# Kernel tuning notes

Hardware: AMD Instinct MI355X
Metric: run time of the kernel (lower is better)

Reference implementation:

```python
import jax, jax.numpy as jnp
import numpy as np

D_MODEL = 1024
NUM_HEADS = 16
HEAD_DIM = D_MODEL // NUM_HEADS  # 64


def setup_inputs() -> dict:
    key = jax.random.key(0)
    k1, k2, k3 = jax.random.split(key, 3)
    x = jax.random.normal(k1, (4, 2048, D_MODEL), dtype=jnp.float32)
    w_qkv = jax.random.normal(k2, (3 * D_MODEL, D_MODEL), dtype=jnp.float32) * 0.02
    b_qkv = jnp.zeros((3 * D_MODEL,), dtype=jnp.float32)
    w_out = jax.random.normal(k3, (D_MODEL, D_MODEL), dtype=jnp.float32) * 0.02
    b_out = jnp.zeros((D_MODEL,), dtype=jnp.float32)
    return {"x": x, "w_qkv": w_qkv, "b_qkv": b_qkv, "w_out": w_out, "b_out": b_out}


def reference(x, w_qkv, b_qkv, w_out, b_out):
    N, S, _ = x.shape
    # qkv projection: (N, S, 3*D) -> (3, N, heads, S, head_dim), matching torch permute(2,0,3,1,4)
    qkv = (jnp.einsum('nsd,ed->nse', x, w_qkv) + b_qkv)
    qkv = qkv.reshape(N, S, 3, NUM_HEADS, HEAD_DIM).transpose(2, 0, 3, 1, 4)
    queries, keys, values = qkv[0], qkv[1], qkv[2]  # each (N, heads, S, head_dim)
    # Faithful to source: einsum labels axis1 as 'q'/'k' and axis2 as 'h',
    # so energy has shape (N, S, heads, heads) -- attention over the heads axis.
    energy = jnp.einsum('nqhd,nkhd->nhqk', queries, keys)
    attention = jax.nn.softmax(energy / jnp.sqrt(jnp.float32(HEAD_DIM)), axis=3)
    out = jnp.einsum('nhql,nlhd->nqhd', attention, values).reshape(N, S, D_MODEL)
    return jnp.einsum('nsd,od->nso', out, w_out) + b_out
```

## Files before the change

### kernel.cpp

```cpp
#include <hip/hip_runtime.h>
#include <hip/hip_bf16.h>


typedef __hip_bfloat16 bf16;
using bf16x8 = __attribute__((ext_vector_type(8))) short;
using f32x4  = __attribute__((ext_vector_type(4))) float;

__device__ __forceinline__ float b2f(unsigned short u) {
    return __uint_as_float(((unsigned)u) << 16);
}
__device__ __forceinline__ unsigned short f2b(float f) {
    bf16 h = __float2bfloat16(f);
    return *reinterpret_cast<unsigned short*>(&h);
}
__device__ __forceinline__ void store1(float* p, float v) { *p = v; }
__device__ __forceinline__ void store1(bf16* p, float v) { *p = __float2bfloat16(v); }

__device__ __forceinline__ void gload_lds16(const bf16* g, bf16* l) {
    __builtin_amdgcn_global_load_lds(
        (const __attribute__((address_space(1))) void*)g,
        (__attribute__((address_space(3))) void*)l, 16, 0, 0);
}

#define BAR()   __builtin_amdgcn_s_barrier()
#define LGKM(N) asm volatile("s_waitcnt lgkmcnt(" #N ")" ::: "memory")
#define VMC(N)  asm volatile("s_waitcnt vmcnt(" #N ")" ::: "memory")

template <typename CT>
__global__ __launch_bounds__(512, 2)
void gemm1b(const bf16* __restrict__ A, const bf16* __restrict__ B,
            const float* __restrict__ bias, CT* __restrict__ C,
            int M, int N, int K, int gx) {
    __shared__ alignas(1024) bf16 smem[3][384 * 64];

    const int t    = threadIdx.x;
    const int lane = t & 63;
    const int wid  = t >> 6;
    const int wr   = wid >> 2;
    const int wc   = wid & 3;

    const int nwg = gridDim.x;
    const int bid = blockIdx.x;
    const int wg  = (bid & 7) * (nwg >> 3) + (bid >> 3);
    const int m0  = (wg / gx) * 128;
    const int n0  = (wg % gx) * 256;

    const int nt = K / 64;

    const int srow = lane >> 3;
    const int kel  = ((lane & 7) ^ (lane >> 3)) * 8;

    auto stageA = [&](int tt) {
        if (tt >= nt) return;
        bf16* lp = &smem[tt % 3][wid * 1024];
        const bf16* gp = A + (size_t)(m0 + wid * 16 + srow) * K + tt * 64 + kel;
        gload_lds16(gp, lp);
        gload_lds16(gp + (size_t)8 * K, lp + 512);
    };
    auto stageB = [&](int tt, int h) {
        if (tt >= nt) return;
        bf16* lp = &smem[tt % 3][8192 + h * 8192 + wid * 1024];
        const bf16* gp = B + (size_t)(n0 + h * 128 + wid * 16 + srow) * K + tt * 64 + kel;
        gload_lds16(gp, lp);
        gload_lds16(gp + (size_t)8 * K, lp + 512);
    };

    const int arow_base = wr * 64 + (lane & 15);
    const int brow_base = wc * 64 + (lane & 15);
    const int kqb       = (lane >> 4) * 16;
    auto LDA = [&](int buf, int kk, int m) -> bf16x8 {
        const int row = arow_base + m * 16;
        const int ab  = row * 128 + ((kk * 64 + kqb) ^ ((row & 7) << 4));
        return *(const bf16x8*)((const char*)&smem[buf][0] + ab);
    };
    auto LDB = [&](int buf, int kk, int n) -> bf16x8 {
        const int row = brow_base + n * 16;
        const int bb  = 16384 + row * 128 + ((kk * 64 + kqb) ^ ((row & 7) << 4));
        return *(const bf16x8*)((const char*)&smem[buf][0] + bb);
    };

    f32x4 acc[4][4] = {};
    bf16x8 af0[4], bf0[4], af1[4], bf1[4];

    stageA(0); stageB(0, 0); stageB(0, 1);
    stageA(1); stageB(1, 0); stageB(1, 1);
    VMC(6);
    BAR();

    for (int tt = 0; tt < nt; ++tt) {
        const int buf = tt % 3;

#pragma unroll
        for (int m = 0; m < 4; ++m) af0[m] = LDA(buf, 0, m);
#pragma unroll
        for (int n = 0; n < 4; ++n) bf0[n] = LDB(buf, 0, n);
#pragma unroll
        for (int m = 0; m < 4; ++m) af1[m] = LDA(buf, 1, m);
#pragma unroll
        for (int n = 0; n < 4; ++n) bf1[n] = LDB(buf, 1, n);
        stageA(tt + 2); stageB(tt + 2, 0); stageB(tt + 2, 1);
        LGKM(8);
        __builtin_amdgcn_s_setprio(1);
#pragma unroll
        for (int m = 0; m < 4; ++m)
#pragma unroll
            for (int n = 0; n < 4; ++n)
                acc[m][n] = __builtin_amdgcn_mfma_f32_16x16x32_bf16(
                    af0[m], bf0[n], acc[m][n], 0, 0, 0);
        __builtin_amdgcn_s_setprio(0);
        LGKM(0);
        __builtin_amdgcn_s_setprio(1);
#pragma unroll
        for (int m = 0; m < 4; ++m)
#pragma unroll
            for (int n = 0; n < 4; ++n)
                acc[m][n] = __builtin_amdgcn_mfma_f32_16x16x32_bf16(
                    af1[m], bf1[n], acc[m][n], 0, 0, 0);
        __builtin_amdgcn_s_setprio(0);
        if (tt < nt - 2) { VMC(6); } else { VMC(0); }
        BAR();
    }

#pragma unroll
    for (int m = 0; m < 4; ++m) {
        const int row = m0 + wr * 64 + m * 16 + (lane >> 4) * 4;
#pragma unroll
        for (int n = 0; n < 4; ++n) {
            const int col = n0 + wc * 64 + n * 16 + (lane & 15);
            const float bval = bias[col];
#pragma unroll
            for (int r = 0; r < 4; ++r)
                store1(&C[(size_t)(row + r) * N + col], acc[m][n][r] + bval);
        }
    }
}

__global__ __launch_bounds__(256)
void cvt2_f32_bf16(const float* __restrict__ in1, bf16* __restrict__ out1, int n1,
                   const float* __restrict__ in2, bf16* __restrict__ out2, int n2) {
    int i = blockIdx.x * 256 + threadIdx.x;
    const float* in;
    bf16* out;
    if (i < n1) { in = in1; out = out1; }
    else        { in = in2; out = out2; i -= n1; if (i >= n2) return; }
    float4 v = ((const float4*)in)[i];
    ushort4 o = {f2b(v.x), f2b(v.y), f2b(v.z), f2b(v.w)};
    ((ushort4*)out)[i] = o;
}

__global__ __launch_bounds__(256)
void cvt_f32_bf16(const float* __restrict__ in, bf16* __restrict__ out, int n4) {
    int i = blockIdx.x * 256 + threadIdx.x;
    if (i >= n4) return;
    float4 v = ((const float4*)in)[i];
    ushort4 o = {f2b(v.x), f2b(v.y), f2b(v.z), f2b(v.w)};
    ((ushort4*)out)[i] = o;
}

__global__ __launch_bounds__(256)
void attn_kernel(const bf16* __restrict__ qkv, bf16* __restrict__ T) {
    __shared__ float lds[4][48 * 68];

    const int wave = threadIdx.x >> 6;
    const int lane = threadIdx.x & 63;
    const int token = blockIdx.x * 4 + wave;
    const int n = token >> 11;
    const int s = token & 2047;

    float* L = lds[wave];
    const bf16* src = qkv + (size_t)token * 3072;

#pragma unroll
    for (int i = 0; i < 6; ++i) {
        int idx = i * 64 + lane;
        uint4 v = *reinterpret_cast<const uint4*>(src + (size_t)idx * 8);
        int e0 = idx * 8;
        float* dst = &L[(e0 >> 6) * 68 + (e0 & 63)];
        float4 a, b;
        a.x = b2f((unsigned short)(v.x & 0xffff));
        a.y = b2f((unsigned short)(v.x >> 16));
        a.z = b2f((unsigned short)(v.y & 0xffff));
        a.w = b2f((unsigned short)(v.y >> 16));
        b.x = b2f((unsigned short)(v.z & 0xffff));
        b.y = b2f((unsigned short)(v.z >> 16));
        b.z = b2f((unsigned short)(v.w & 0xffff));
        b.w = b2f((unsigned short)(v.w >> 16));
        *(float4*)dst = a;
        *(float4*)(dst + 4) = b;
    }
    __syncthreads();

    const int q0 = lane & 15;
    const int g  = lane >> 4;

    float e[4] = {0.f, 0.f, 0.f, 0.f};
    const float* Qr = &L[q0 * 68];
    const float* K0 = &L[(16 + g * 4) * 68];
#pragma unroll
    for (int d = 0; d < 64; d += 4) {
        float4 q4 = *(const float4*)(Qr + d);
#pragma unroll
        for (int j = 0; j < 4; ++j) {
            float4 k4 = *(const float4*)(K0 + j * 68 + d);
            e[j] += q4.x * k4.x + q4.y * k4.y + q4.z * k4.z + q4.w * k4.w;
        }
    }
#pragma unroll
    for (int j = 0; j < 4; ++j) e[j] *= 0.125f;

    float m = fmaxf(fmaxf(e[0], e[1]), fmaxf(e[2], e[3]));
    m = fmaxf(m, __shfl_xor(m, 16));
    m = fmaxf(m, __shfl_xor(m, 32));
    float p[4], sum = 0.f;
#pragma unroll
    for (int j = 0; j < 4; ++j) { p[j] = __expf(e[j] - m); sum += p[j]; }
    sum += __shfl_xor(sum, 16);
    sum += __shfl_xor(sum, 32);
    const float inv = 1.0f / sum;

    float prow[16];
#pragma unroll
    for (int j = 0; j < 4; ++j) {
        prow[g * 4 + j]         = p[j] * inv;
        prow[((g ^ 1) * 4) + j] = __shfl_xor(p[j], 16) * inv;
        prow[((g ^ 2) * 4) + j] = __shfl_xor(p[j], 32) * inv;
        prow[((g ^ 3) * 4) + j] = __shfl_xor(p[j], 48) * inv;
    }

    const int d0 = g * 16;
    float4 o4[4] = {};
#pragma unroll
    for (int k = 0; k < 16; ++k) {
        const float p1 = prow[k];
        const float* Vr = &L[(32 + k) * 68 + d0];
#pragma unroll
        for (int c = 0; c < 4; ++c) {
            float4 v = *(const float4*)(Vr + c * 4);
            o4[c].x += p1 * v.x; o4[c].y += p1 * v.y;
            o4[c].z += p1 * v.z; o4[c].w += p1 * v.w;
        }
    }
    unsigned short outv[16];
#pragma unroll
    for (int c = 0; c < 4; ++c) {
        outv[c * 4 + 0] = f2b(o4[c].x); outv[c * 4 + 1] = f2b(o4[c].y);
        outv[c * 4 + 2] = f2b(o4[c].z); outv[c * 4 + 3] = f2b(o4[c].w);
    }
    const int sp = q0 * 128 + (s >> 4);
    size_t off = ((size_t)n * 2048 + sp) * 1024 + (size_t)(s & 15) * 64 + d0;
    uint4* dst = reinterpret_cast<uint4*>(T + off);
    const uint4* sv = reinterpret_cast<const uint4*>(outv);
    dst[0] = sv[0];
    dst[1] = sv[1];
}

extern "C" void kernel_launch(void* const* d_in, const int* in_sizes, int n_in,
                              void* d_out, int out_size, void* d_ws, size_t ws_size,
                              hipStream_t stream) {
    const float* x     = (const float*)d_in[0];
    const float* w_qkv = (const float*)d_in[1];
    const float* b_qkv = (const float*)d_in[2];
    const float* w_out = (const float*)d_in[3];
    const float* b_out = (const float*)d_in[4];
    float* out = (float*)d_out;

    const int M = 8192, E = 3072, K = 1024, D = 1024;

    bf16* qkv = (bf16*)d_ws;
    bf16* T   = qkv + (size_t)M * E;
    bf16* W2b = qkv;
    bf16* W1b = (bf16*)d_out;
    bf16* X16 = W1b + (size_t)E * K;

    dim3 blk(256);
    const int n1 = M * K / 4, n2 = E * K / 4;

    cvt2_f32_bf16<<<dim3((n1 + n2) / 256), blk, 0, stream>>>(
        x, X16, n1, w_qkv, W1b, n2);
    gemm1b<bf16><<<dim3((M / 128) * (E / 256)), dim3(512), 0, stream>>>(
        X16, W1b, b_qkv, qkv, M, E, K, E / 256);
    attn_kernel<<<dim3(M / 4), blk, 0, stream>>>(qkv, T);
    cvt_f32_bf16<<<dim3(D * K / 4 / 256), blk, 0, stream>>>(w_out, W2b, D * K / 4);
    gemm1b<float><<<dim3((M / 128) * (D / 256)), dim3(512), 0, stream>>>(
        T, W2b, b_out, out, M, D, K, D / 256);
}
```

Measured before the change: 124.1 us.

## Add 128x384 tile GEMM kernel for the QKV projection

Adds a dedicated GEMM kernel with a 128x384 output tile and two-stage LDS double buffering, and uses it for the QKV projection in place of the 128x256 triple-buffered kernel. Each wave now computes a 64x96 sub-tile (4x6 MFMA blocks), which raises arithmetic intensity per LDS load and cuts the block count from 768 to 512. The cost is 128KB of LDS per block and more accumulator registers. With 512 blocks on 256 CUs the work divides into even waves, but occupancy may fall, and the shallower pipeline exposes more load latency.

```diff
diff --git a/kernel.cpp b/kernel.cpp
--- a/kernel.cpp
+++ b/kernel.cpp
@@ -25,6 +25,116 @@
 #define BAR()   __builtin_amdgcn_s_barrier()
 #define LGKM(N) asm volatile("s_waitcnt lgkmcnt(" #N ")" ::: "memory")
 #define VMC(N)  asm volatile("s_waitcnt vmcnt(" #N ")" ::: "memory")
+
+__global__ __launch_bounds__(512, 2)
+void gemm384(const bf16* __restrict__ A, const bf16* __restrict__ B,
+             const float* __restrict__ bias, bf16* __restrict__ C,
+             int M, int N, int K, int gx) {
+    __shared__ alignas(1024) bf16 smem[2][512 * 64];
+
+    const int t    = threadIdx.x;
+    const int lane = t & 63;
+    const int wid  = t >> 6;
+    const int wr   = wid >> 2;
+    const int wc   = wid & 3;
+
+    const int nwg = gridDim.x;
+    const int bid = blockIdx.x;
+    const int wg  = (bid & 7) * (nwg >> 3) + (bid >> 3);
+    const int m0  = (wg / gx) * 128;
+    const int n0  = (wg % gx) * 384;
+    const int nt  = K / 64;
+
+    const int srow = lane >> 3;
+    const int kel  = ((lane & 7) ^ (lane >> 3)) * 8;
+
+    auto stageA = [&](int tt) {
+        if (tt >= nt) return;
+        bf16* lp = &smem[tt & 1][wid * 1024];
+        const bf16* gp = A + (size_t)(m0 + wid * 16 + srow) * K + tt * 64 + kel;
+        gload_lds16(gp, lp);
+        gload_lds16(gp + (size_t)8 * K, lp + 512);
+    };
+    auto stageB = [&](int tt) {
+        if (tt >= nt) return;
+        bf16* lp = &smem[tt & 1][8192 + wid * 3072];
+        const bf16* gp = B + (size_t)(n0 + wid * 48 + srow) * K + tt * 64 + kel;
+#pragma unroll
+        for (int i = 0; i < 6; ++i)
+            gload_lds16(gp + (size_t)(i * 8) * K, lp + i * 512);
+    };
+
+    const int arow_base = wr * 64 + (lane & 15);
+    const int brow_base = wc * 96 + (lane & 15);
+    const int kqb       = (lane >> 4) * 16;
+    auto LDA = [&](int buf, int kk, int m) -> bf16x8 {
+        const int row = arow_base + m * 16;
+        const int ab  = row * 128 + ((kk * 64 + kqb) ^ ((row & 7) << 4));
+        return *(const bf16x8*)((const char*)&smem[buf][0] + ab);
+    };
+    auto LDB = [&](int buf, int kk, int n) -> bf16x8 {
+        const int row = brow_base + n * 16;
+        const int bb  = 16384 + row * 128 + ((kk * 64 + kqb) ^ ((row & 7) << 4));
+        return *(const bf16x8*)((const char*)&smem[buf][0] + bb);
+    };
+
+    f32x4 acc[4][6] = {};
+    bf16x8 af0[4], bv0[6], af1[4], bv1[6];
+
+    stageA(0); stageB(0);
+    VMC(0);
+    BAR();
+
+    for (int tt = 0; tt < nt; ++tt) {
+        const int buf = tt & 1;
+
+        stageA(tt + 1); stageB(tt + 1);
+
+#pragma unroll
+        for (int m = 0; m < 4; ++m) af0[m] = LDA(buf, 0, m);
+#pragma unroll
+        for (int n = 0; n < 6; ++n) bv0[n] = LDB(buf, 0, n);
+#pragma unroll
+        for (int m = 0; m < 4; ++m) af1[m] = LDA(buf, 1, m);
+#pragma unroll
+        for (int n = 0; n < 6; ++n) bv1[n] = LDB(buf, 1, n);
+
+        LGKM(10);
+        __builtin_amdgcn_s_setprio(1);
+#pragma unroll
+        for (int m = 0; m < 4; ++m)
+#pragma unroll
+            for (int n = 0; n < 6; ++n)
+                acc[m][n] = __builtin_amdgcn_mfma_f32_16x16x32_bf16(
+                    af0[m], bv0[n], acc[m][n], 0, 0, 0);
+        __builtin_amdgcn_s_setprio(0);
+        LGKM(0);
+        __builtin_amdgcn_s_setprio(1);
+#pragma unroll
+        for (int m = 0; m < 4; ++m)
+#pragma unroll
+            for (int n = 0; n < 6; ++n)
+                acc[m][n] = __builtin_amdgcn_mfma_f32_16x16x32_bf16(
+                    af1[m], bv1[n], acc[m][n], 0, 0, 0);
+        __builtin_amdgcn_s_setprio(0);
+
+        VMC(0);
+        BAR();
+    }
+
+#pragma unroll
+    for (int m = 0; m < 4; ++m) {
+        const int row = m0 + wr * 64 + m * 16 + (lane >> 4) * 4;
+#pragma unroll
+        for (int n = 0; n < 6; ++n) {
+            const int col = n0 + wc * 96 + n * 16 + (lane & 15);
+            const float bval = bias[col];
+#pragma unroll
+            for (int r = 0; r < 4; ++r)
+                store1(&C[(size_t)(row + r) * N + col], acc[m][n][r] + bval);
+        }
+    }
+}
 
 template <typename CT>
 __global__ __launch_bounds__(512, 2)
@@ -44,8 +154,7 @@
     const int wg  = (bid & 7) * (nwg >> 3) + (bid >> 3);
     const int m0  = (wg / gx) * 128;
     const int n0  = (wg % gx) * 256;
-
-    const int nt = K / 64;
+    const int nt  = K / 64;
 
     const int srow = lane >> 3;
     const int kel  = ((lane & 7) ^ (lane >> 3)) * 8;
@@ -277,8 +386,8 @@
 
     cvt2_f32_bf16<<<dim3((n1 + n2) / 256), blk, 0, stream>>>(
         x, X16, n1, w_qkv, W1b, n2);
-    gemm1b<bf16><<<dim3((M / 128) * (E / 256)), dim3(512), 0, stream>>>(
-        X16, W1b, b_qkv, qkv, M, E, K, E / 256);
+    gemm384<<<dim3((M / 128) * (E / 384)), dim3(512), 0, stream>>>(
+        X16, W1b, b_qkv, qkv, M, E, K, E / 384);
     attn_kernel<<<dim3(M / 4), blk, 0, stream>>>(qkv, T);
     cvt_f32_bf16<<<dim3(D * K / 4 / 256), blk, 0, stream>>>(w_out, W2b, D * K / 4);
     gemm1b<float><<<dim3((M / 128) * (D / 256)), dim3(512), 0, stream>>>(
```

New measurement: 116.9 us. 5.8% less time.

## Widen QKV GEMM tile to 128x384 and switch to double-buffered LDS

Applied to the files above, without the earlier changes.

The GEMM kernel is templated on the number of N fragments per wave. The QKV projection now uses 128x384 tiles, which cuts the grid to 512 blocks, while the output projection keeps 128x256. The LDS pipeline drops from a 3-stage ring with a two-tile lookahead to a 2-stage double buffer that waits for all global loads every iteration. The wider tile improves operand reuse and wave balance, but the full vmcnt wait each iteration exposes more global-load latency and the extra accumulators add register pressure.

```diff
diff --git a/kernel.cpp b/kernel.cpp
--- a/kernel.cpp
+++ b/kernel.cpp
@@ -26,12 +26,12 @@
 #define LGKM(N) asm volatile("s_waitcnt lgkmcnt(" #N ")" ::: "memory")
 #define VMC(N)  asm volatile("s_waitcnt vmcnt(" #N ")" ::: "memory")
 
-template <typename CT>
+template <int NF, typename CT>
 __global__ __launch_bounds__(512, 2)
-void gemm1b(const bf16* __restrict__ A, const bf16* __restrict__ B,
+void gemm_u(const bf16* __restrict__ A, const bf16* __restrict__ B,
             const float* __restrict__ bias, CT* __restrict__ C,
             int M, int N, int K, int gx) {
-    __shared__ alignas(1024) bf16 smem[3][384 * 64];
+    __shared__ alignas(1024) bf16 smem[2][(128 + 64 * NF) * 64];
 
     const int t    = threadIdx.x;
     const int lane = t & 63;
@@ -43,30 +43,30 @@
     const int bid = blockIdx.x;
     const int wg  = (bid & 7) * (nwg >> 3) + (bid >> 3);
     const int m0  = (wg / gx) * 128;
-    const int n0  = (wg % gx) * 256;
-
-    const int nt = K / 64;
+    const int n0  = (wg % gx) * (64 * NF);
+    const int nt  = K / 64;
 
     const int srow = lane >> 3;
     const int kel  = ((lane & 7) ^ (lane >> 3)) * 8;
 
     auto stageA = [&](int tt) {
         if (tt >= nt) return;
-        bf16* lp = &smem[tt % 3][wid * 1024];
+        bf16* lp = &smem[tt & 1][wid * 1024];
         const bf16* gp = A + (size_t)(m0 + wid * 16 + srow) * K + tt * 64 + kel;
         gload_lds16(gp, lp);
         gload_lds16(gp + (size_t)8 * K, lp + 512);
     };
-    auto stageB = [&](int tt, int h) {
+    auto stageB = [&](int tt) {
         if (tt >= nt) return;
-        bf16* lp = &smem[tt % 3][8192 + h * 8192 + wid * 1024];
-        const bf16* gp = B + (size_t)(n0 + h * 128 + wid * 16 + srow) * K + tt * 64 + kel;
-        gload_lds16(gp, lp);
-        gload_lds16(gp + (size_t)8 * K, lp + 512);
+        bf16* lp = &smem[tt & 1][8192 + wid * (NF * 512)];
+        const bf16* gp = B + (size_t)(n0 + wid * 8 * NF + srow) * K + tt * 64 + kel;
+#pragma unroll
+        for (int i = 0; i < NF; ++i)
+            gload_lds16(gp + (size_t)(i * 8) * K, lp + i * 512);
     };
 
     const int arow_base = wr * 64 + (lane & 15);
-    const int brow_base = wc * 64 + (lane & 15);
+    const int brow_base = wc * (16 * NF) + (lane & 15);
     const int kqb       = (lane >> 4) * 16;
     auto LDA = [&](int buf, int kk, int m) -> bf16x8 {
         const int row = arow_base + m * 16;
@@ -79,45 +79,47 @@
         return *(const bf16x8*)((const char*)&smem[buf][0] + bb);
     };
 
-    f32x4 acc[4][4] = {};
-    bf16x8 af0[4], bf0[4], af1[4], bf1[4];
-
-    stageA(0); stageB(0, 0); stageB(0, 1);
-    stageA(1); stageB(1, 0); stageB(1, 1);
-    VMC(6);
+    f32x4 acc[4][NF] = {};
+    bf16x8 af0[4], bv0[NF], af1[4], bv1[NF];
+
+    stageA(0); stageB(0);
+    VMC(0);
     BAR();
 
     for (int tt = 0; tt < nt; ++tt) {
-        const int buf = tt % 3;
+        const int buf = tt & 1;
 
 #pragma unroll
         for (int m = 0; m < 4; ++m) af0[m] = LDA(buf, 0, m);
 #pragma unroll
-        for (int n = 0; n < 4; ++n) bf0[n] = LDB(buf, 0, n);
+        for (int n = 0; n < NF; ++n) bv0[n] = LDB(buf, 0, n);
 #pragma unroll
         for (int m = 0; m < 4; ++m) af1[m] = LDA(buf, 1, m);
 #pragma unroll
-        for (int n = 0; n < 4; ++n) bf1[n] = LDB(buf, 1, n);
-        stageA(tt + 2); stageB(tt + 2, 0); stageB(tt + 2, 1);
-        LGKM(8);
+        for (int n = 0; n < NF; ++n) bv1[n] = LDB(buf, 1, n);
+
+        stageA(tt + 1); stageB(tt + 1);
+
+        if constexpr (NF == 6) { LGKM(10); } else { LGKM(8); }
         __builtin_amdgcn_s_setprio(1);
 #pragma unroll
         for (int m = 0; m < 4; ++m)
 #pragma unroll
-            for (int n = 0; n < 4; ++n)
+            for (int n = 0; n < NF; ++n)
                 acc[m][n] = __builtin_amdgcn_mfma_f32_16x16x32_bf16(
-                    af0[m], bf0[n], acc[m][n], 0, 0, 0);
+                    af0[m], bv0[n], acc[m][n], 0, 0, 0);
         __builtin_amdgcn_s_setprio(0);
         LGKM(0);
         __builtin_amdgcn_s_setprio(1);
 #pragma unroll
         for (int m = 0; m < 4; ++m)
 #pragma unroll
-            for (int n = 0; n < 4; ++n)
+            for (int n = 0; n < NF; ++n)
                 acc[m][n] = __builtin_amdgcn_mfma_f32_16x16x32_bf16(
-                    af1[m], bf1[n], acc[m][n], 0, 0, 0);
+                    af1[m], bv1[n], acc[m][n], 0, 0, 0);
         __builtin_amdgcn_s_setprio(0);
-        if (tt < nt - 2) { VMC(6); } else { VMC(0); }
+
+        VMC(0);
         BAR();
     }
 
@@ -125,8 +127,8 @@
     for (int m = 0; m < 4; ++m) {
         const int row = m0 + wr * 64 + m * 16 + (lane >> 4) * 4;
 #pragma unroll
-        for (int n = 0; n < 4; ++n) {
-            const int col = n0 + wc * 64 + n * 16 + (lane & 15);
+        for (int n = 0; n < NF; ++n) {
+            const int col = n0 + wc * (16 * NF) + n * 16 + (lane & 15);
             const float bval = bias[col];
 #pragma unroll
             for (int r = 0; r < 4; ++r)
@@ -277,10 +279,10 @@
 
     cvt2_f32_bf16<<<dim3((n1 + n2) / 256), blk, 0, stream>>>(
         x, X16, n1, w_qkv, W1b, n2);
-    gemm1b<bf16><<<dim3((M / 128) * (E / 256)), dim3(512), 0, stream>>>(
-        X16, W1b, b_qkv, qkv, M, E, K, E / 256);
+    gemm_u<6, bf16><<<dim3((M / 128) * (E / 384)), dim3(512), 0, stream>>>(
+        X16, W1b, b_qkv, qkv, M, E, K, E / 384);
     attn_kernel<<<dim3(M / 4), blk, 0, stream>>>(qkv, T);
     cvt_f32_bf16<<<dim3(D * K / 4 / 256), blk, 0, stream>>>(w_out, W2b, D * K / 4);
-    gemm1b<float><<<dim3((M / 128) * (D / 256)), dim3(512), 0, stream>>>(
+    gemm_u<4, float><<<dim3((M / 128) * (D / 256)), dim3(512), 0, stream>>>(
         T, W2b, b_out, out, M, D, K, D / 256);
 }
```

Measured after the change: 116.6 us. 6.0% less time.
